# Optimization experiments

Hardware: AMD Instinct MI355X
Metric: run time of the kernel (lower is better)

## Reference

```python
import jax, jax.numpy as jnp
import numpy as np

B, S, D, H, DFF = 2, 4096, 512, 8, 2048
DK = D // H
EPS = 1e-5


def layer_norm(x, g, b):
    mu = jnp.mean(x, axis=-1, keepdims=True)
    var = jnp.mean((x - mu) ** 2, axis=-1, keepdims=True)
    return (x - mu) * jax.lax.rsqrt(var + EPS) * g + b


def setup_inputs() -> dict:
    key = jax.random.key(0)
    ks = jax.random.split(key, 12)
    s = 1.0 / np.sqrt(D)
    return {
        "x": jax.random.normal(ks[0], (B, S, D), jnp.float32),
        "mask": jnp.ones((B, 1, 1, S), jnp.int32),
        "wq": jax.random.normal(ks[1], (D, D), jnp.float32) * s,
        "wk": jax.random.normal(ks[2], (D, D), jnp.float32) * s,
        "wv": jax.random.normal(ks[3], (D, D), jnp.float32) * s,
        "wo": jax.random.normal(ks[4], (D, D), jnp.float32) * s,
        "w1": jax.random.normal(ks[5], (D, DFF), jnp.float32) * s,
        "b1": jnp.zeros((DFF,), jnp.float32),
        "w2": jax.random.normal(ks[6], (DFF, D), jnp.float32) * (1.0 / np.sqrt(DFF)),
        "b2": jnp.zeros((D,), jnp.float32),
        "g1": jnp.ones((D,), jnp.float32),
        "be1": jnp.zeros((D,), jnp.float32),
        "g2": jnp.ones((D,), jnp.float32),
        "be2": jnp.zeros((D,), jnp.float32),
    }


def reference(x, mask, wq, wk, wv, wo, w1, b1, w2, b2, g1, be1, g2, be2):
    # projections -> [B, H, S, DK]
    def split_heads(t):
        return t.reshape(B, S, H, DK).transpose(0, 2, 1, 3)

    q = split_heads(x @ wq)
    k = split_heads(x @ wk)
    v = split_heads(x @ wv)

    scores = jnp.einsum("bhqd,bhkd->bhqk", q, k) / np.sqrt(DK)
    scores = jnp.where(mask == 0, -1e9, scores)
    attn = jax.nn.softmax(scores, axis=-1)  # dropout=0 (eval)
    ctx = jnp.einsum("bhqk,bhkd->bhqd", attn, v)
    ctx = ctx.transpose(0, 2, 1, 3).reshape(B, S, D)
    attn_out = ctx @ wo

    x1 = layer_norm(x + attn_out, g1, be1)
    ff = jax.nn.relu(x1 @ w1 + b1) @ w2 + b2
    return layer_norm(x1 + ff, g2, be2)
```

## Files before the change

kernel.cpp:

```cpp
#include <hip/hip_runtime.h>
#include <hip/hip_bf16.h>


typedef unsigned short u16;
typedef unsigned int u32;
typedef __attribute__((ext_vector_type(2))) u32 u32x2;
typedef __attribute__((ext_vector_type(4))) u16 u16x4;
typedef __attribute__((ext_vector_type(8))) u16 u16x8;
typedef __attribute__((ext_vector_type(2))) float f32x2;
typedef __attribute__((ext_vector_type(4))) float f32x4;
typedef __attribute__((ext_vector_type(16))) float f32x16;
typedef __attribute__((ext_vector_type(8))) short bf16x8;

#define CB 2
#define CS 4096
#define CD 512
#define CH 8
#define CDK 64
#define CDFF 2048
#define NXC ((size_t)CB * CS * CD)
#define NSP 2
#define BH (CB * CH)
#define BHS (BH * CS)

__device__ __forceinline__ float bf2f(u16 u) {
    union { u32 i; float f; } c;
    c.i = ((u32)u) << 16;
    return c.f;
}

__device__ __forceinline__ u16 f2bf(float f) {
    u32 x = __float_as_uint(f);
    u32 r = (x + 0x7fffu + ((x >> 16) & 1u)) >> 16;
    return (u16)r;
}

__device__ __forceinline__ u32 packbf2(float a, float b) {
    __hip_bfloat162 h = __float22bfloat162_rn(float2{a, b});
    union { __hip_bfloat162 h; u32 u; } c;
    c.h = h;
    return c.u;
}

__device__ __forceinline__ void dma16(const u16* g, u16* l) {
    __builtin_amdgcn_global_load_lds(
        (const __attribute__((address_space(1))) void*)g,
        (__attribute__((address_space(3))) void*)l, 16, 0, 0);
}

__global__ void detect_dtype(const u32* __restrict__ xw, int* __restrict__ flag) {
    __shared__ int red[256];
    int sane = 0;
    for (int i = threadIdx.x; i < 2048; i += 256) {
        u32 w = xw[i];
        u32 lo = w & 0xFFFFu;
        u32 e = (lo >> 7) & 0xFFu;
        if (lo == 0u || lo == 0x8000u || (e >= 96u && e <= 159u)) sane++;
    }
    red[threadIdx.x] = sane;
    __syncthreads();
    for (int s = 128; s > 0; s >>= 1) {
        if ((int)threadIdx.x < s) red[threadIdx.x] += red[threadIdx.x + s];
        __syncthreads();
    }
    if (threadIdx.x == 0) *flag = (red[0] >= 1843) ? 1 : 0;
}

__global__ __launch_bounds__(256) void convert_bf16(
    const void* __restrict__ src, u16* __restrict__ dst, int n,
    const int* __restrict__ flag)
{
    const bool isbf = (*flag != 0);
    const int n8 = n >> 3;
    int i = blockIdx.x * 256 + threadIdx.x;
    const int stride = gridDim.x * 256;
    if (isbf) {
        const u16x8* s = (const u16x8*)src;
        u16x8* d = (u16x8*)dst;
        for (; i < n8; i += stride) d[i] = s[i];
    } else {
        const f32x4* s = (const f32x4*)src;
        for (; i < n8; i += stride) {
            f32x4 a = s[2 * i];
            f32x4 b = s[2 * i + 1];
            u16x8 o;
#pragma unroll
            for (int e = 0; e < 4; e++) {
                o[e] = f2bf(a[e]);
                o[4 + e] = f2bf(b[e]);
            }
            *(u16x8*)&dst[(size_t)i * 8] = o;
        }
    }
    if (blockIdx.x == 0 && threadIdx.x == 0) {
        for (int r = n8 * 8; r < n; r++) {
            if (isbf) dst[r] = ((const u16*)src)[r];
            else dst[r] = f2bf(((const float*)src)[r]);
        }
    }
}

struct PrepArgs {
    const void* tsrc[6];
    u16* tdst[6];
    int R[6], Cc[6], nbx[6];
    int cum[7];
    const int* mask;
    unsigned long long* bits;
    const void* ssrc[6];
    u16* sdst[6];
    int sn[6];
};

__global__ __launch_bounds__(256) void prep_all(PrepArgs pa, const int* __restrict__ flag) {
    const int bid = blockIdx.x;
    const int tid = threadIdx.x;
    if (bid < pa.cum[6]) {
        __shared__ float t[32][33];
        int w = 0;
#pragma unroll
        for (int k = 1; k < 6; k++) w += (bid >= pa.cum[k]) ? 1 : 0;
        const int local = bid - pa.cum[w];
        const int nbx = pa.nbx[w];
        const int bx = local % nbx;
        const int by = local / nbx;
        const int R = pa.R[w];
        const int Cc = pa.Cc[w];
        const void* src = pa.tsrc[w];
        u16* dst = pa.tdst[w];
        const bool isbf = (*flag != 0);
        const int r0 = by * 32;
        const int c0 = bx * 32;
        const int col = tid & 31;
        const int row = tid >> 5;
#pragma unroll
        for (int it = 0; it < 4; it++) {
            int rr = row + it * 8;
            float v;
            if (isbf) v = bf2f(((const u16*)src)[(size_t)(r0 + rr) * Cc + c0 + col]);
            else v = ((const float*)src)[(size_t)(r0 + rr) * Cc + c0 + col];
            t[rr][col] = v;
        }
        __syncthreads();
#pragma unroll
        for (int it = 0; it < 4; it++) {
            int rr = row + it * 8;
            dst[(size_t)(c0 + rr) * R + r0 + col] = f2bf(t[col][rr]);
        }
    } else if (bid < pa.cum[6] + 32) {
        const int local = bid - pa.cum[6];
        int w = local * 4 + (tid >> 6);
        int lane = tid & 63;
        int b = w >> 6, t = w & 63;
        int val = pa.mask[b * CS + t * 64 + lane];
        unsigned long long bal = __ballot(val != 0);
        if (lane == 0) pa.bits[w] = bal;
    } else {
        const bool isbf = (*flag != 0);
        for (int t = 0; t < 6; t++) {
            for (int i = tid; i < pa.sn[t]; i += 256) {
                if (isbf) pa.sdst[t][i] = ((const u16*)pa.ssrc[t])[i];
                else pa.sdst[t][i] = f2bf(((const float*)pa.ssrc[t])[i]);
            }
        }
    }
}

#define F_SPLIT 1
#define F_BIAS  2
#define F_RELU  4

template <int FLAGS>
__global__ __launch_bounds__(256, 3) void gemm_mfma(
    const u16* __restrict__ A, const u16* __restrict__ Bt,
    const u16* __restrict__ bias, u16* __restrict__ C,
    int M, int N, int K)
{
    __shared__ u16 AS[8192];
    __shared__ u16 BS[8192];

    const int tid = threadIdx.x;
    const int lane = tid & 63;
    const int wave = tid >> 6;
    const int lrow = lane & 15;
    const int quad = lane >> 4;
    const int rswg = lrow & 7;
    const int wm = wave & 1;
    const int wn = wave >> 1;
    const int m0 = blockIdx.y * 128;
    const int n0 = blockIdx.x * 128;

    const u16* Aps[4];
    const u16* Bps[4];
    u16* Adst[4];
    u16* Bdst[4];
#pragma unroll
    for (int r = 0; r < 4; r++) {
        const int idx = r * 256 + tid;
        const int row = idx >> 3;
        const int g = (idx & 7) ^ (row & 7);
        Aps[r] = A + (size_t)(m0 + row) * K + g * 8;
        Bps[r] = Bt + (size_t)(n0 + row) * K + g * 8;
        Adst[r] = &AS[r * 2048 + wave * 512];
        Bdst[r] = &BS[r * 2048 + wave * 512];
    }

    f32x4 acc[4][4];
#pragma unroll
    for (int i = 0; i < 4; i++)
#pragma unroll
        for (int j = 0; j < 4; j++) acc[i][j] = f32x4{0.f, 0.f, 0.f, 0.f};

    const char* As8 = (const char*)&AS[0];
    const char* Bs8 = (const char*)&BS[0];

    for (int k0 = 0; k0 < K; k0 += 64) {
        __syncthreads();
#pragma unroll
        for (int r = 0; r < 4; r++) {
            dma16(Aps[r] + k0, Adst[r]);
            dma16(Bps[r] + k0, Bdst[r]);
        }
        __syncthreads();

#pragma unroll
        for (int kk = 0; kk < 2; kk++) {
            bf16x8 af[4], bfr[4];
#pragma unroll
            for (int i = 0; i < 4; i++) {
                const int row = wm * 64 + i * 16 + lrow;
                af[i] = *(const bf16x8*)(As8 + row * 128 +
                                         (((kk * 4 + quad) ^ rswg) << 4));
            }
#pragma unroll
            for (int j = 0; j < 4; j++) {
                const int row = wn * 64 + j * 16 + lrow;
                bfr[j] = *(const bf16x8*)(Bs8 + row * 128 +
                                          (((kk * 4 + quad) ^ rswg) << 4));
            }
#pragma unroll
            for (int i = 0; i < 4; i++)
#pragma unroll
                for (int j = 0; j < 4; j++)
                    acc[i][j] = __builtin_amdgcn_mfma_f32_16x16x32_bf16(
                        af[i], bfr[j], acc[i][j], 0, 0, 0);
        }
    }

    const int mbase = m0 + wm * 64;
    const int nbase = n0 + wn * 64;
#pragma unroll
    for (int i = 0; i < 4; i++) {
#pragma unroll
        for (int j = 0; j < 4; j++) {
            const int n = nbase + j * 16 + lrow;
            if ((FLAGS & F_SPLIT) && ((nbase + j * 16) >> 9) == 2) {
                const int dk = n & 63;
                const int h = (n >> 6) & 7;
                const int sb = mbase + i * 16 + quad * 4;
                const int bb = sb >> 12;
                const int ss = sb & 4095;
                u16x4 ov;
#pragma unroll
                for (int r = 0; r < 4; r++) ov[r] = f2bf(acc[i][j][r]);
                *(u16x4*)&C[2 * NXC + (((size_t)(bb * CH + h)) * CDK + dk) * CS + ss] = ov;
            } else {
#pragma unroll
                for (int r = 0; r < 4; r++) {
                    const int m = mbase + i * 16 + quad * 4 + r;
                    float val = acc[i][j][r];
                    if (FLAGS & F_BIAS) val += bf2f(bias[n]);
                    if (FLAGS & F_RELU) val = fmaxf(val, 0.f);
                    if (FLAGS & F_SPLIT) {
                        const int proj = n >> 9;
                        const int d = n & 511;
                        const int h = d >> 6;
                        const int dk = d & 63;
                        const int bb = m >> 12;
                        const int ss = m & 4095;
                        C[proj * NXC + (((size_t)(bb * CH + h)) * CS + ss) * CDK + dk] = f2bf(val);
                    } else {
                        C[(size_t)m * N + n] = f2bf(val);
                    }
                }
            }
        }
    }
}

__global__ __launch_bounds__(256, 4) void mfma_attn2(
    const u16* __restrict__ Qb, const u16* __restrict__ Kb,
    const u16* __restrict__ Vt, const unsigned long long* __restrict__ bits,
    u16* __restrict__ pOT, float* __restrict__ Ls)
{
    __shared__ u16 KB[3][4096];
    __shared__ u16 VB[2][4096];

    const int tid = threadIdx.x;
    const int lane = tid & 63;
    const int wave = tid >> 6;
    const int qcol = lane & 31;
    const int hf = lane >> 5;

    const int bh = blockIdx.y;
    const int b = bh >> 3;
    const int z = blockIdx.z;
    const int q0 = blockIdx.x * 128 + wave * 32;

    const float SC = 0.125f * 1.44269504088896340736f;

    bf16x8 bq[4];
    const u16* qp = Qb + ((size_t)bh * CS + q0 + qcol) * CDK + hf * 8;
#pragma unroll
    for (int c = 0; c < 4; c++) {
        bf16x8 raw = *(const bf16x8*)(qp + c * 16);
        union { u32 u[4]; bf16x8 v; } cv;
#pragma unroll
        for (int j = 0; j < 4; j++)
            cv.u[j] = packbf2(bf2f((u16)raw[2 * j]) * SC, bf2f((u16)raw[2 * j + 1]) * SC);
        bq[c] = cv.v;
    }

    f32x4 z4 = {0.f, 0.f, 0.f, 0.f};
    asm volatile("" : "+v"(z4));
    f32x16 zero16;
#pragma unroll
    for (int i = 0; i < 16; i++) zero16[i] = z4[i & 3];

    f32x16 ot[2];
#pragma unroll
    for (int dt = 0; dt < 2; dt++)
#pragma unroll
        for (int i = 0; i < 16; i++) ot[dt][i] = 0.f;
    float lh = 0.f;

    const u16* kbase = Kb + (size_t)bh * CS * CDK;
    const u16* vbase = Vt + (size_t)bh * CDK * CS;
    const unsigned long long* bp = bits + b * 64;

    const int t0 = z * (CS / NSP);
    const int t1 = t0 + (CS / NSP);

    const int rsw = qcol & 7;
    int koff[2][4];
#pragma unroll
    for (int rt = 0; rt < 2; rt++)
#pragma unroll
        for (int c = 0; c < 4; c++)
            koff[rt][c] = ((rt * 32 + qcol) * 64 + (((2 * c + hf) ^ rsw) * 8)) * 2;
    const char* kb0 = (const char*)&KB[0][0];
    const char* vb0 = (const char*)&VB[0][0];

    const int w2 = wave * 2;

#define STAGE_K(KOFFB, t)                                                    \
    {                                                                        \
        const u16* kb_ = kbase + (size_t)(t) * CDK;                          \
        _Pragma("unroll")                                                    \
        for (int n = 0; n < 2; n++) {                                        \
            int idx = (w2 + n) * 64 + lane;                                  \
            int row = idx >> 3;                                              \
            int g = (idx & 7) ^ (row & 7);                                   \
            dma16(kb_ + row * CDK + g * 8,                                   \
                  (u16*)((char*)&KB[0][0] + (KOFFB) + (w2 + n) * 1024));     \
        }                                                                    \
    }
#define STAGE_V(P, t)                                                        \
    {                                                                        \
        const u16* vb_ = vbase + (t);                                        \
        _Pragma("unroll")                                                    \
        for (int n = 0; n < 2; n++) {                                        \
            int idx = (w2 + n) * 64 + lane;                                  \
            int row = idx >> 3;                                              \
            int g = (idx & 7) ^ (row & 7);                                   \
            dma16(vb_ + (size_t)row * CS + g * 8,                            \
                  (u16*)((char*)&VB[0][0] + (P) * 8192 + (w2 + n) * 1024));  \
        }                                                                    \
    }

#define TBODY(KROFF, VOFF, BM, MASKED, MIDSYNC)                              \
    {                                                                        \
        f32x2 racc = {0.f, 0.f};                                             \
        _Pragma("unroll")                                                    \
        for (int mt = 0; mt < 2; mt++) {                                     \
            f32x16 s;                                                        \
            _Pragma("unroll")                                                \
            for (int c = 0; c < 4; c++) {                                    \
                bf16x8 ak = *(const bf16x8*)(kb0 + (KROFF) + koff[mt][c]);   \
                s = __builtin_amdgcn_mfma_f32_32x32x16_bf16(                 \
                    ak, bq[c], (c == 0) ? zero16 : s, 0, 0, 0);              \
            }                                                                \
            if (MASKED) {                                                    \
                const unsigned long long bm_ = (BM);                         \
                if (bm_ != ~0ull) {                                          \
                    _Pragma("unroll")                                        \
                    for (int i = 0; i < 16; i++) {                           \
                        const int key = (i & 3) + 8 * (i >> 2) + 4 * hf + 32 * mt; \
                        if (!((bm_ >> key) & 1ull)) s[i] = -1e30f;           \
                    }                                                        \
                }                                                            \
            }                                                                \
            u32 pk[8];                                                       \
            _Pragma("unroll")                                                \
            for (int g = 0; g < 4; g++) {                                    \
                float p0 = __builtin_amdgcn_exp2f(s[4 * g + 0]);             \
                float p1 = __builtin_amdgcn_exp2f(s[4 * g + 1]);             \
                float p2 = __builtin_amdgcn_exp2f(s[4 * g + 2]);             \
                float p3 = __builtin_amdgcn_exp2f(s[4 * g + 3]);             \
                racc += f32x2{p0, p1};                                       \
                racc += f32x2{p2, p3};                                       \
                pk[2 * g + 0] = packbf2(p0, p1);                             \
                pk[2 * g + 1] = packbf2(p2, p3);                             \
            }                                                                \
            if (mt == 0) { MIDSYNC }                                         \
            _Pragma("unroll")                                                \
            for (int cc = 0; cc < 2; cc++) {                                 \
                u32x2 r0 = __builtin_amdgcn_permlane32_swap(                 \
                    pk[4 * cc + 0], pk[4 * cc + 2], false, false);           \
                u32x2 r1 = __builtin_amdgcn_permlane32_swap(                 \
                    pk[4 * cc + 1], pk[4 * cc + 3], false, false);           \
                union { u32 u[4]; bf16x8 v; } pf;                            \
                pf.u[0] = r0.x;                                              \
                pf.u[1] = r1.x;                                              \
                pf.u[2] = r0.y;                                              \
                pf.u[3] = r1.y;                                              \
                const int c = 2 * mt + cc;                                   \
                _Pragma("unroll")                                            \
                for (int dt = 0; dt < 2; dt++) {                             \
                    bf16x8 av = *(const bf16x8*)(vb0 + (VOFF) + koff[dt][c]); \
                    ot[dt] = __builtin_amdgcn_mfma_f32_32x32x16_bf16(        \
                        av, pf.v, ot[dt], 0, 0, 0);                          \
                }                                                            \
            }                                                                \
        }                                                                    \
        lh += racc.x + racc.y;                                               \
    }

#define FTILE(P, TT, KR, KS, DOV, DOK, TOPASM, MIDASM)                       \
    {                                                                        \
        asm volatile(TOPASM ::: "memory");                                   \
        __builtin_amdgcn_sched_barrier(0);                                   \
        __builtin_amdgcn_s_barrier();                                        \
        __builtin_amdgcn_sched_barrier(0);                                   \
        if (DOV) STAGE_V((P) ^ 1, (TT) + 64);                                \
        if (DOK) STAGE_K((KS), (TT) + 128);                                  \
        TBODY((KR), (P) * 8192, 0ull, 0,                                     \
              asm volatile(MIDASM ::: "memory");                             \
              __builtin_amdgcn_sched_barrier(0);                             \
              __builtin_amdgcn_s_barrier();                                  \
              __builtin_amdgcn_sched_barrier(0);)                            \
    }

    unsigned long long am = ~0ull;
    const int tb0 = t0 >> 6;
    for (int i = 0; i < 32; i++) am &= bp[tb0 + i];
    const bool allones = (am == ~0ull);

    if (allones) {
        STAGE_K(0, t0);
        STAGE_V(0, t0);
        STAGE_K(8192, t0 + 64);

        u32 kr = 0;
        for (int m = 0; m < 15; m++) {
            const int t = t0 + m * 128;
            const u32 kr1 = (kr == 16384u) ? 0u : kr + 8192u;
            const u32 ks0 = (kr1 == 16384u) ? 0u : kr1 + 8192u;
            FTILE(0, t, kr, ks0, 1, 1,
                  "s_waitcnt vmcnt(4)", "s_waitcnt vmcnt(6)")
            FTILE(1, t + 64, kr1, kr, 1, 1,
                  "s_waitcnt vmcnt(4)", "s_waitcnt vmcnt(6)")
            kr = ks0;
        }
        {
            const int t = t0 + 30 * 64;
            const u32 kr1 = (kr == 16384u) ? 0u : kr + 8192u;
            FTILE(0, t, kr, 0, 1, 0,
                  "s_waitcnt vmcnt(4)", "s_waitcnt vmcnt(4)")
            FTILE(1, t + 64, kr1, 0, 0, 0,
                  "s_waitcnt vmcnt(2)", "s_waitcnt vmcnt(0)")
        }
    } else {
        STAGE_K(0, t0);
        STAGE_V(0, t0);
        __syncthreads();
        for (int t = t0; t < t1; t += 64) {
            const int p = (t >> 6) & 1;
            const u32 kro = (u32)p * 8192u;
            if (t + 64 < t1) {
                STAGE_V(p ^ 1, t + 64);
                STAGE_K((p ^ 1) * 8192, t + 64);
            }
            TBODY(kro, p * 8192, bp[t >> 6], 1, ;)
            __syncthreads();
        }
    }
#undef FTILE
#undef TBODY
#undef STAGE_V
#undef STAGE_K

    u32x2 rr = __builtin_amdgcn_permlane32_swap(
        __float_as_uint(lh), __float_as_uint(lh), false, false);
    const float l = lh + __uint_as_float(hf ? rr.x : rr.y);

    const int q_lin = bh * CS + q0 + qcol;
    if (hf == 0) Ls[z * BHS + q_lin] = l;
    const size_t pbase = ((size_t)(z * BH + bh) * CDK) * CS + q0 + qcol;
#pragma unroll
    for (int dt = 0; dt < 2; dt++)
#pragma unroll
        for (int i = 0; i < 16; i++) {
            const int dk = (i & 3) + 8 * (i >> 2) + 4 * hf + 32 * dt;
            pOT[pbase + (size_t)dk * CS] = f2bf(ot[dt][i]);
        }
}

__global__ __launch_bounds__(256) void attn_combine(
    const u16* __restrict__ pOT, const float* __restrict__ Ls,
    u16* __restrict__ ctx)
{
    __shared__ float linv[64];
    __shared__ u16 T[64][72];

    const int bh = blockIdx.y;
    const int s0 = blockIdx.x * 64;
    const int b = bh >> 3, h = bh & 7;
    const int tid = threadIdx.x;

    if (tid < 64) {
        float L = 0.f;
#pragma unroll
        for (int z = 0; z < NSP; z++) L += Ls[z * BHS + bh * CS + s0 + tid];
        linv[tid] = (L > 0.f) ? 1.f / L : 0.f;
    }
    __syncthreads();

    const int dk = tid >> 2;
    const int sc = (tid & 3) * 16;
    float acc[16] = {};
#pragma unroll
    for (int z = 0; z < NSP; z++) {
        const u16* p = pOT + ((size_t)(z * BH + bh) * CDK + dk) * CS + s0 + sc;
        u16x8 v0 = *(const u16x8*)p;
        u16x8 v1 = *(const u16x8*)(p + 8);
#pragma unroll
        for (int e = 0; e < 8; e++) {
            acc[e] += bf2f(v0[e]);
            acc[8 + e] += bf2f(v1[e]);
        }
    }
#pragma unroll
    for (int e = 0; e < 16; e++)
        T[sc + e][dk] = f2bf(acc[e] * linv[sc + e]);
    __syncthreads();

    const int sr = tid >> 2;
    const int dc = (tid & 3) * 16;
    u16x8 o0, o1;
#pragma unroll
    for (int e = 0; e < 8; e++) {
        o0[e] = T[sr][dc + e];
        o1[e] = T[sr][dc + 8 + e];
    }
    u16* cp = &ctx[((size_t)b * CS + s0 + sr) * CD + h * CDK + dc];
    *(u16x8*)cp = o0;
    *(u16x8*)(cp + 8) = o1;
}

__global__ __launch_bounds__(256) void ln_kernel(
    const u16* __restrict__ xa, const u16* __restrict__ xb,
    const u16* __restrict__ g, const u16* __restrict__ be,
    u16* __restrict__ outb, float* __restrict__ outf,
    const int* __restrict__ flag)
{
    const int lane = threadIdx.x & 63;
    const int wave = threadIdx.x >> 6;
    const size_t row = (size_t)blockIdx.x * 4 + wave;
    const int c0 = lane * 8;

    u16x8 av = *(const u16x8*)(xa + row * CD + c0);
    u16x8 bv = *(const u16x8*)(xb + row * CD + c0);

    float v[8];
    float s1 = 0.f, s2 = 0.f;
#pragma unroll
    for (int e = 0; e < 8; e++) {
        v[e] = bf2f(av[e]) + bf2f(bv[e]);
        s1 += v[e];
        s2 += v[e] * v[e];
    }
#pragma unroll
    for (int off = 32; off > 0; off >>= 1) {
        s1 += __shfl_xor(s1, off, 64);
        s2 += __shfl_xor(s2, off, 64);
    }
    const float mu = s1 * (1.f / CD);
    const float var = fmaxf(s2 * (1.f / CD) - mu * mu, 0.f);
    const float r = rsqrtf(var + 1e-5f);

    u16x8 gv = *(const u16x8*)(g + c0);
    u16x8 ev = *(const u16x8*)(be + c0);
    float res[8];
#pragma unroll
    for (int e = 0; e < 8; e++)
        res[e] = (v[e] - mu) * r * bf2f(gv[e]) + bf2f(ev[e]);

    const int flg = *flag;
    const bool f32out = (outf != nullptr) && (flg == 0);
    if (f32out) {
        float4 o0 = make_float4(res[0], res[1], res[2], res[3]);
        float4 o1 = make_float4(res[4], res[5], res[6], res[7]);
        *(float4*)(outf + row * CD + c0) = o0;
        *(float4*)(outf + row * CD + c0 + 4) = o1;
    } else {
        u16x8 ov;
#pragma unroll
        for (int e = 0; e < 8; e++) ov[e] = f2bf(res[e]);
        *(u16x8*)(outb + row * CD + c0) = ov;
    }
}


extern "C" void kernel_launch(void* const* d_in, const int* in_sizes, int n_in,
                              void* d_out, int out_size, void* d_ws, size_t ws_size,
                              hipStream_t stream)
{
    const void* x_raw   = d_in[0];
    const int*  mask    = (const int*)d_in[1];
    const void* wq_raw  = d_in[2];
    const void* wk_raw  = d_in[3];
    const void* wv_raw  = d_in[4];
    const void* wo_raw  = d_in[5];
    const void* w1_raw  = d_in[6];
    const void* b1_raw  = d_in[7];
    const void* w2_raw  = d_in[8];
    const void* b2_raw  = d_in[9];
    const void* g1_raw  = d_in[10];
    const void* be1_raw = d_in[11];
    const void* g2_raw  = d_in[12];
    const void* be2_raw = d_in[13];

    const size_t NX = NXC;
    const size_t WSZ = (size_t)CD * CD;
    const size_t W1SZ = (size_t)CD * CDFF;

    u16* ws = (u16*)d_ws;
    int* flag = (int*)d_ws;
    unsigned long long* bits = (unsigned long long*)(ws + 512);
    u16* base = ws + 1024;
    u16* xc  = base;
    u16* q   = base + 1 * NX;
    u16* k   = base + 2 * NX;
    u16* v   = base + 3 * NX;
    u16* ctx = base + 4 * NX;
    u16* att = base + 5 * NX;
    u16* x1  = base + 6 * NX;
    u16* ffo = base + 7 * NX;
    u16* ffh = base + 8 * NX;
    u16* wt  = base + 12 * NX;
    u16* wqkvT = wt;
    u16* woT = wqkvT + 3 * WSZ;
    u16* w1T = woT + WSZ;
    u16* w2T = w1T + W1SZ;
    u16* b1c = w2T + W1SZ;
    u16* b2c = b1c + CDFF;
    u16* g1c = b2c + CD;
    u16* be1c = g1c + CD;
    u16* g2c = be1c + CD;
    u16* be2c = g2c + CD;
    u16* wend = be2c + CD;

    const size_t need = (size_t)(wend - ws) * sizeof(u16);
    if (ws_size < need) return;
    (void)k;

    u16* pOT = ffh;
    float* Ls = (float*)att;

    detect_dtype<<<1, 256, 0, stream>>>((const u32*)x_raw, flag);

    convert_bf16<<<1024, 256, 0, stream>>>(x_raw, xc, (int)NX, flag);

    PrepArgs pa;
    pa.tsrc[0] = wq_raw; pa.tdst[0] = wqkvT;           pa.R[0] = CD;   pa.Cc[0] = CD;
    pa.tsrc[1] = wk_raw; pa.tdst[1] = wqkvT + WSZ;     pa.R[1] = CD;   pa.Cc[1] = CD;
    pa.tsrc[2] = wv_raw; pa.tdst[2] = wqkvT + 2 * WSZ; pa.R[2] = CD;   pa.Cc[2] = CD;
    pa.tsrc[3] = wo_raw; pa.tdst[3] = woT;             pa.R[3] = CD;   pa.Cc[3] = CD;
    pa.tsrc[4] = w1_raw; pa.tdst[4] = w1T;             pa.R[4] = CD;   pa.Cc[4] = CDFF;
    pa.tsrc[5] = w2_raw; pa.tdst[5] = w2T;             pa.R[5] = CDFF; pa.Cc[5] = CD;
    int cum = 0;
    for (int w = 0; w < 6; w++) {
        pa.nbx[w] = pa.Cc[w] / 32;
        pa.cum[w] = cum;
        cum += (pa.Cc[w] / 32) * (pa.R[w] / 32);
    }
    pa.cum[6] = cum;
    pa.mask = mask;
    pa.bits = bits;
    pa.ssrc[0] = b1_raw;  pa.sdst[0] = b1c;  pa.sn[0] = CDFF;
    pa.ssrc[1] = b2_raw;  pa.sdst[1] = b2c;  pa.sn[1] = CD;
    pa.ssrc[2] = g1_raw;  pa.sdst[2] = g1c;  pa.sn[2] = CD;
    pa.ssrc[3] = be1_raw; pa.sdst[3] = be1c; pa.sn[3] = CD;
    pa.ssrc[4] = g2_raw;  pa.sdst[4] = g2c;  pa.sn[4] = CD;
    pa.ssrc[5] = be2_raw; pa.sdst[5] = be2c; pa.sn[5] = CD;
    prep_all<<<cum + 32 + 1, 256, 0, stream>>>(pa, flag);

    const int M = CB * CS;

    gemm_mfma<F_SPLIT><<<dim3(1536 / 128, M / 128), 256, 0, stream>>>(
        xc, wqkvT, nullptr, q, M, 1536, CD);

    mfma_attn2<<<dim3(CS / 128, BH, NSP), 256, 0, stream>>>(q, k, v, bits, pOT, Ls);
    attn_combine<<<dim3(CS / 64, BH), 256, 0, stream>>>(pOT, Ls, ctx);

    gemm_mfma<0><<<dim3(CD / 128, M / 128), 256, 0, stream>>>(
        ctx, woT, nullptr, att, M, CD, CD);

    ln_kernel<<<dim3(M / 4), 256, 0, stream>>>(xc, att, g1c, be1c, x1, nullptr, flag);

    gemm_mfma<F_BIAS | F_RELU><<<dim3(CDFF / 128, M / 128), 256, 0, stream>>>(
        x1, w1T, b1c, ffh, M, CDFF, CD);
    gemm_mfma<F_BIAS><<<dim3(CD / 128, M / 128), 256, 0, stream>>>(
        ffh, w2T, b2c, ffo, M, CD, CDFF);

    ln_kernel<<<dim3(M / 4), 256, 0, stream>>>(x1, ffo, g2c, be2c,
                                               (u16*)d_out, (float*)d_out, flag);
}
```

Before: 315.6 us.

## Add triple-buffered GEMM pipeline and LDS-staged vectorized epilogue stores

Adds a PIPE variant of the MFMA GEMM with a 3-stage LDS ring buffer, BK=32, explicit vmcnt waits and a single barrier per k-step. This lets global-to-LDS DMA overlap with MFMA compute for the narrow-N GEMMs (Wo projection and FFN down-projection), which launch only 256 blocks. All GEMMs also get a new epilogue that stages results through LDS, so stores are 16-byte vectorized instead of scattered 2-byte writes, and the bias is loaded once per column. The pipelined variant uses more LDS and is limited to one block per CU. The unswizzled 32-wide LDS rows may cause bank conflicts.

```diff
diff --git a/kernel.cpp b/kernel.cpp
--- a/kernel.cpp
+++ b/kernel.cpp
@@ -170,119 +170,194 @@
 #define F_BIAS  2
 #define F_RELU  4
 
-template <int FLAGS>
-__global__ __launch_bounds__(256, 3) void gemm_mfma(
+template <int FLAGS, int PIPE>
+__global__ __launch_bounds__(256, PIPE ? 1 : 3) void gemm_mfma(
     const u16* __restrict__ A, const u16* __restrict__ Bt,
     const u16* __restrict__ bias, u16* __restrict__ C,
     int M, int N, int K)
 {
-    __shared__ u16 AS[8192];
-    __shared__ u16 BS[8192];
+    constexpr int ABn = PIPE ? 12288 : 8192;
+    __shared__ __align__(16) u16 POOL[2 * ABn + 4 * 1536];
+    u16* ASb = POOL;
+    u16* BSb = POOL + ABn;
 
     const int tid = threadIdx.x;
     const int lane = tid & 63;
     const int wave = tid >> 6;
     const int lrow = lane & 15;
     const int quad = lane >> 4;
-    const int rswg = lrow & 7;
     const int wm = wave & 1;
     const int wn = wave >> 1;
     const int m0 = blockIdx.y * 128;
     const int n0 = blockIdx.x * 128;
 
-    const u16* Aps[4];
-    const u16* Bps[4];
-    u16* Adst[4];
-    u16* Bdst[4];
-#pragma unroll
-    for (int r = 0; r < 4; r++) {
-        const int idx = r * 256 + tid;
-        const int row = idx >> 3;
-        const int g = (idx & 7) ^ (row & 7);
-        Aps[r] = A + (size_t)(m0 + row) * K + g * 8;
-        Bps[r] = Bt + (size_t)(n0 + row) * K + g * 8;
-        Adst[r] = &AS[r * 2048 + wave * 512];
-        Bdst[r] = &BS[r * 2048 + wave * 512];
-    }
-
     f32x4 acc[4][4];
 #pragma unroll
     for (int i = 0; i < 4; i++)
 #pragma unroll
         for (int j = 0; j < 4; j++) acc[i][j] = f32x4{0.f, 0.f, 0.f, 0.f};
 
-    const char* As8 = (const char*)&AS[0];
-    const char* Bs8 = (const char*)&BS[0];
-
-    for (int k0 = 0; k0 < K; k0 += 64) {
-        __syncthreads();
+    if constexpr (PIPE) {
+        const int idx0 = wave * 128 + lane;
+        const int idx1 = idx0 + 64;
+        const u16* Ap0 = A + (size_t)(m0 + (idx0 >> 2)) * K + (idx0 & 3) * 8;
+        const u16* Ap1 = A + (size_t)(m0 + (idx1 >> 2)) * K + (idx1 & 3) * 8;
+        const u16* Bp0 = Bt + (size_t)(n0 + (idx0 >> 2)) * K + (idx0 & 3) * 8;
+        const u16* Bp1 = Bt + (size_t)(n0 + (idx1 >> 2)) * K + (idx1 & 3) * 8;
+        const int NK = K >> 5;
+
+#define PSTAGE(BOFF, KOFF)                                                   \
+        {                                                                    \
+            dma16(Ap0 + (KOFF), ASb + (BOFF) + wave * 1024);                 \
+            dma16(Ap1 + (KOFF), ASb + (BOFF) + wave * 1024 + 512);           \
+            dma16(Bp0 + (KOFF), BSb + (BOFF) + wave * 1024);                 \
+            dma16(Bp1 + (KOFF), BSb + (BOFF) + wave * 1024 + 512);           \
+        }
+        PSTAGE(0, 0)
+        PSTAGE(4096, 32)
+        u32 bR = 0;
+        for (int j = 0; j < NK; j++) {
+            if (j < NK - 1) { asm volatile("s_waitcnt vmcnt(4)" ::: "memory"); }
+            else            { asm volatile("s_waitcnt vmcnt(0)" ::: "memory"); }
+            __builtin_amdgcn_sched_barrier(0);
+            __builtin_amdgcn_s_barrier();
+            __builtin_amdgcn_sched_barrier(0);
+            if (j + 2 < NK) {
+                u32 bS = bR + 8192;
+                if (bS >= 12288) bS -= 12288;
+                PSTAGE(bS, (j + 2) * 32)
+            }
+            bf16x8 af[4], bfr[4];
+#pragma unroll
+            for (int i = 0; i < 4; i++)
+                af[i] = *(const bf16x8*)&ASb[bR + (wm * 64 + i * 16 + lrow) * 32 + quad * 8];
+#pragma unroll
+            for (int jj = 0; jj < 4; jj++)
+                bfr[jj] = *(const bf16x8*)&BSb[bR + (wn * 64 + jj * 16 + lrow) * 32 + quad * 8];
+#pragma unroll
+            for (int i = 0; i < 4; i++)
+#pragma unroll
+                for (int jj = 0; jj < 4; jj++)
+                    acc[i][jj] = __builtin_amdgcn_mfma_f32_16x16x32_bf16(
+                        af[i], bfr[jj], acc[i][jj], 0, 0, 0);
+            bR = (bR == 8192u) ? 0u : bR + 4096u;
+        }
+#undef PSTAGE
+    } else {
+        const int rswg = lrow & 7;
+        const u16* Aps[4];
+        const u16* Bps[4];
+        u16* Adst[4];
+        u16* Bdst[4];
 #pragma unroll
         for (int r = 0; r < 4; r++) {
-            dma16(Aps[r] + k0, Adst[r]);
-            dma16(Bps[r] + k0, Bdst[r]);
-        }
-        __syncthreads();
-
-#pragma unroll
-        for (int kk = 0; kk < 2; kk++) {
-            bf16x8 af[4], bfr[4];
-#pragma unroll
-            for (int i = 0; i < 4; i++) {
-                const int row = wm * 64 + i * 16 + lrow;
-                af[i] = *(const bf16x8*)(As8 + row * 128 +
-                                         (((kk * 4 + quad) ^ rswg) << 4));
+            const int idx = r * 256 + tid;
+            const int row = idx >> 3;
+            const int g = (idx & 7) ^ (row & 7);
+            Aps[r] = A + (size_t)(m0 + row) * K + g * 8;
+            Bps[r] = Bt + (size_t)(n0 + row) * K + g * 8;
+            Adst[r] = &ASb[r * 2048 + wave * 512];
+            Bdst[r] = &BSb[r * 2048 + wave * 512];
+        }
+        const char* As8 = (const char*)ASb;
+        const char* Bs8 = (const char*)BSb;
+
+        for (int k0 = 0; k0 < K; k0 += 64) {
+            __syncthreads();
+#pragma unroll
+            for (int r = 0; r < 4; r++) {
+                dma16(Aps[r] + k0, Adst[r]);
+                dma16(Bps[r] + k0, Bdst[r]);
             }
-#pragma unroll
-            for (int j = 0; j < 4; j++) {
-                const int row = wn * 64 + j * 16 + lrow;
-                bfr[j] = *(const bf16x8*)(Bs8 + row * 128 +
-                                          (((kk * 4 + quad) ^ rswg) << 4));
+            __syncthreads();
+
+#pragma unroll
+            for (int kk = 0; kk < 2; kk++) {
+                bf16x8 af[4], bfr[4];
+#pragma unroll
+                for (int i = 0; i < 4; i++) {
+                    const int row = wm * 64 + i * 16 + lrow;
+                    af[i] = *(const bf16x8*)(As8 + row * 128 +
+                                             (((kk * 4 + quad) ^ rswg) << 4));
+                }
+#pragma unroll
+                for (int j = 0; j < 4; j++) {
+                    const int row = wn * 64 + j * 16 + lrow;
+                    bfr[j] = *(const bf16x8*)(Bs8 + row * 128 +
+                                              (((kk * 4 + quad) ^ rswg) << 4));
+                }
+#pragma unroll
+                for (int i = 0; i < 4; i++)
+#pragma unroll
+                    for (int j = 0; j < 4; j++)
+                        acc[i][j] = __builtin_amdgcn_mfma_f32_16x16x32_bf16(
+                            af[i], bfr[j], acc[i][j], 0, 0, 0);
             }
-#pragma unroll
-            for (int i = 0; i < 4; i++)
-#pragma unroll
-                for (int j = 0; j < 4; j++)
-                    acc[i][j] = __builtin_amdgcn_mfma_f32_16x16x32_bf16(
-                        af[i], bfr[j], acc[i][j], 0, 0, 0);
-        }
-    }
-
+        }
+    }
+
+    u16* st = POOL + 2 * ABn + wave * 1536;
     const int mbase = m0 + wm * 64;
     const int nbase = n0 + wn * 64;
-#pragma unroll
-    for (int i = 0; i < 4; i++) {
-#pragma unroll
-        for (int j = 0; j < 4; j++) {
-            const int n = nbase + j * 16 + lrow;
-            if ((FLAGS & F_SPLIT) && ((nbase + j * 16) >> 9) == 2) {
-                const int dk = n & 63;
-                const int h = (n >> 6) & 7;
-                const int sb = mbase + i * 16 + quad * 4;
-                const int bb = sb >> 12;
-                const int ss = sb & 4095;
-                u16x4 ov;
-#pragma unroll
-                for (int r = 0; r < 4; r++) ov[r] = f2bf(acc[i][j][r]);
-                *(u16x4*)&C[2 * NXC + (((size_t)(bb * CH + h)) * CDK + dk) * CS + ss] = ov;
-            } else {
+    const int msub = mbase & 4095;
+    const int bb = mbase >> 12;
+    const bool vpath = (FLAGS & F_SPLIT) && ((nbase >> 9) == 2);
+
+    if (vpath) {
+        const int h = (nbase >> 6) & 7;
+        u16* vdst = C + 2 * NXC + (((size_t)(bb * CH + h)) * CDK) * CS;
+#pragma unroll
+        for (int i = 0; i < 4; i++) {
+#pragma unroll
+            for (int j = 0; j < 4; j++)
+#pragma unroll
+                for (int r = 0; r < 4; r++)
+                    st[(j * 16 + lrow) * 24 + quad * 4 + r] = f2bf(acc[i][j][r]);
+#pragma unroll
+            for (int rr = 0; rr < 2; rr++) {
+                const int idx = rr * 64 + lane;
+                const int dk = idx >> 1;
+                const int sch = idx & 1;
+                u16x8 val = *(const u16x8*)&st[dk * 24 + sch * 8];
+                *(u16x8*)&vdst[(size_t)dk * CS + msub + i * 16 + sch * 8] = val;
+            }
+        }
+    } else {
+        float bv[4];
+        if (FLAGS & F_BIAS) {
+#pragma unroll
+            for (int j = 0; j < 4; j++) bv[j] = bf2f(bias[nbase + j * 16 + lrow]);
+        }
+        const int proj = nbase >> 9;
+        const int h = (nbase >> 6) & 7;
+        u16* qkdst = C + (size_t)proj * NXC + (((size_t)(bb * CH + h)) * CS) * CDK;
+#pragma unroll
+        for (int i = 0; i < 4; i++) {
+#pragma unroll
+            for (int j = 0; j < 4; j++)
 #pragma unroll
                 for (int r = 0; r < 4; r++) {
-                    const int m = mbase + i * 16 + quad * 4 + r;
                     float val = acc[i][j][r];
-                    if (FLAGS & F_BIAS) val += bf2f(bias[n]);
+                    if (FLAGS & F_BIAS) val += bv[j];
                     if (FLAGS & F_RELU) val = fmaxf(val, 0.f);
-                    if (FLAGS & F_SPLIT) {
-                        const int proj = n >> 9;
-                        const int d = n & 511;
-                        const int h = d >> 6;
-                        const int dk = d & 63;
-                        const int bb = m >> 12;
-                        const int ss = m & 4095;
-                        C[proj * NXC + (((size_t)(bb * CH + h)) * CS + ss) * CDK + dk] = f2bf(val);
-                    } else {
-                        C[(size_t)m * N + n] = f2bf(val);
-                    }
+                    st[(quad * 4 + r) * 68 + j * 16 + lrow] = f2bf(val);
                 }
+#pragma unroll
+            for (int rr = 0; rr < 2; rr++) {
+                const int idx = rr * 64 + lane;
+                const int row = idx >> 3;
+                const int ch = idx & 7;
+                u16x4 lo = *(const u16x4*)&st[row * 68 + ch * 8];
+                u16x4 hi = *(const u16x4*)&st[row * 68 + ch * 8 + 4];
+                u16x8 val;
+#pragma unroll
+                for (int e = 0; e < 4; e++) { val[e] = lo[e]; val[4 + e] = hi[e]; }
+                u16* p;
+                if (FLAGS & F_SPLIT)
+                    p = qkdst + (size_t)(msub + i * 16 + row) * CDK + ch * 8;
+                else
+                    p = C + (size_t)(mbase + i * 16 + row) * N + nbase + ch * 8;
+                *(u16x8*)p = val;
             }
         }
     }
@@ -708,20 +783,20 @@
 
     const int M = CB * CS;
 
-    gemm_mfma<F_SPLIT><<<dim3(1536 / 128, M / 128), 256, 0, stream>>>(
+    gemm_mfma<F_SPLIT, 0><<<dim3(1536 / 128, M / 128), 256, 0, stream>>>(
         xc, wqkvT, nullptr, q, M, 1536, CD);
 
     mfma_attn2<<<dim3(CS / 128, BH, NSP), 256, 0, stream>>>(q, k, v, bits, pOT, Ls);
     attn_combine<<<dim3(CS / 64, BH), 256, 0, stream>>>(pOT, Ls, ctx);
 
-    gemm_mfma<0><<<dim3(CD / 128, M / 128), 256, 0, stream>>>(
+    gemm_mfma<0, 1><<<dim3(CD / 128, M / 128), 256, 0, stream>>>(
         ctx, woT, nullptr, att, M, CD, CD);
 
     ln_kernel<<<dim3(M / 4), 256, 0, stream>>>(xc, att, g1c, be1c, x1, nullptr, flag);
 
-    gemm_mfma<F_BIAS | F_RELU><<<dim3(CDFF / 128, M / 128), 256, 0, stream>>>(
+    gemm_mfma<F_BIAS | F_RELU, 0><<<dim3(CDFF / 128, M / 128), 256, 0, stream>>>(
         x1, w1T, b1c, ffh, M, CDFF, CD);
-    gemm_mfma<F_BIAS><<<dim3(CD / 128, M / 128), 256, 0, stream>>>(
+    gemm_mfma<F_BIAS, 1><<<dim3(CD / 128, M / 128), 256, 0, stream>>>(
         ffh, w2T, b2c, ffo, M, CD, CDFF);
 
     ln_kernel<<<dim3(M / 4), 256, 0, stream>>>(x1, ffo, g2c, be2c,
```

Measured after the change: 312.4 us. No clear change (-1.0%).
